# Kernel optimization log

Hardware: AMD Instinct MI355X
Metric: run time of the kernel (lower is better)

## Reference

```python
import jax, jax.numpy as jnp
import numpy as np

B, S, E, H = 2, 2048, 1024, 16
HD = E // H


def setup_inputs() -> dict:
    key = jax.random.key(0)
    ks = jax.random.split(key, 5)
    scale = 1.0 / np.sqrt(E)
    return {
        "query": jax.random.normal(ks[0], (B, S, E), jnp.float32),
        "key": jax.random.normal(ks[1], (B, S, E), jnp.float32),
        "value": jax.random.normal(ks[2], (B, S, E), jnp.float32),
        "qkv_w": jax.random.normal(ks[3], (3 * E, E), jnp.float32) * scale,
        "qkv_b": jnp.zeros((3 * E,), jnp.float32),
        "out_w": jax.random.normal(ks[4], (E, E), jnp.float32) * scale,
        "out_b": jnp.zeros((E,), jnp.float32),
    }


def reference(query, key, value, qkv_w, qkv_b, out_w, out_b):
    # Fused QKV projection from query (module ignores key/value contents)
    qkv = query @ qkv_w.T + qkv_b                      # [B,S,3E]
    qkv = qkv.reshape(B, S, 3, H, HD)
    q = qkv[:, :, 0].transpose(0, 2, 1, 3)             # [B,H,S,HD]
    k = qkv[:, :, 1].transpose(0, 2, 1, 3)
    v = qkv[:, :, 2].transpose(0, 2, 1, 3)
    scaling = 1.0 / np.sqrt(HD)
    scores = jnp.einsum("bhqd,bhkd->bhqk", q, k) * scaling  # [B,H,S,S]
    probs = jax.nn.softmax(scores, axis=-1)
    ctx = jnp.einsum("bhqk,bhkd->bhqd", probs, v)      # [B,H,S,HD]
    ctx = ctx.transpose(0, 2, 1, 3).reshape(B, S, E)
    return ctx @ out_w.T + out_b
```

## Files before the change

kernel.cpp:

```cpp
#include <hip/hip_runtime.h>
#include <hip/hip_bf16.h>
#include <math.h>

#define BB 2
#define SS 2048
#define EE 1024
#define HH 16
#define HD 64

typedef __bf16 bf16;
typedef __bf16 bf16x8 __attribute__((ext_vector_type(8)));
typedef float floatx4 __attribute__((ext_vector_type(4)));
typedef float floatx16 __attribute__((ext_vector_type(16)));

#define MFMA(a, b, c) __builtin_amdgcn_mfma_f32_16x16x32_bf16(a, b, c, 0, 0, 0)
#define MFMA32(a, b, c) __builtin_amdgcn_mfma_f32_32x32x16_bf16(a, b, c, 0, 0, 0)

__device__ inline void async16(const bf16* g, bf16* l) {
    __builtin_amdgcn_global_load_lds(
        (const __attribute__((address_space(1))) void*)g,
        (__attribute__((address_space(3))) void*)l, 16, 0, 0);
}

__device__ inline unsigned cvt_pk_bf16(float a, float b) {
    unsigned r;
    asm("v_cvt_pk_bf16_f32 %0, %1, %2" : "=v"(r) : "v"(a), "v"(b));
    return r;
}

__device__ inline float fast_exp2(float x) {
    float r;
    asm("v_exp_f32 %0, %1" : "=v"(r) : "v"(x));
    return r;
}

__global__ __launch_bounds__(256) void cvt3(
    const float* __restrict__ a, const float* __restrict__ b,
    const float* __restrict__ c,
    bf16* __restrict__ oa, bf16* __restrict__ ob, bf16* __restrict__ oc) {
    const long NA = (long)4096 * 1024, NB = (long)3072 * 1024, NC = (long)1024 * 1024;
    const long total = (NA + NB + NC) >> 2;
    long i = (long)blockIdx.x * blockDim.x + threadIdx.x;
    const long stride = (long)gridDim.x * blockDim.x;
    for (; i < total; i += stride) {
        const long e = i << 2;
        const float* src;
        bf16* dst;
        if (e < NA)           { src = a + e;            dst = oa + e; }
        else if (e < NA + NB) { src = b + (e - NA);     dst = ob + (e - NA); }
        else                  { src = c + (e - NA - NB); dst = oc + (e - NA - NB); }
        float4 v = *(const float4*)src;
        union { bf16 h[4]; uint2 u; } t;
        t.h[0] = (bf16)v.x; t.h[1] = (bf16)v.y; t.h[2] = (bf16)v.z; t.h[3] = (bf16)v.w;
        *(uint2*)dst = t.u;
    }
}

__global__ __launch_bounds__(256) void qkv_gemm(
    const bf16* __restrict__ A, const bf16* __restrict__ W,
    const float* __restrict__ bias,
    bf16* __restrict__ Qw, bf16* __restrict__ Kw, bf16* __restrict__ Vtw) {
    __shared__ __align__(16) bf16 As[2][128 * 64];
    __shared__ __align__(16) bf16 Bs[2][128 * 64];
    const int tid  = threadIdx.x;
    const int wave = tid >> 6, lane = tid & 63;
    const int quad = lane >> 4, l16 = lane & 15;
    const int wr = wave >> 1, wc = wave & 1;
    const int m0 = blockIdx.y * 128, n0 = blockIdx.x * 128;
    const int lr = lane >> 3;
    const int lcs = ((lane & 7) ^ (lr & 7)) * 8;
    const int rsw = (l16 & 7) << 3;

    const bf16* Ag = A + (long)(m0 + wave * 32 + lr) * 1024 + lcs;
    const bf16* Bg = W + (long)(n0 + wave * 32 + lr) * 1024 + lcs;
    const int lbase = (wave * 32) * 64 + lane * 8;

    floatx4 acc[4][4] = {};

#pragma unroll
    for (int j = 0; j < 4; ++j) {
        async16(Ag + (long)j * 8 * 1024, &As[0][lbase + j * 8 * 64]);
        async16(Bg + (long)j * 8 * 1024, &Bs[0][lbase + j * 8 * 64]);
    }

    for (int ks = 0; ks < 16; ++ks) {
        __syncthreads();
        const int cur = ks & 1;
        if (ks < 15) {
            const int nxt = cur ^ 1, k0 = (ks + 1) * 64;
#pragma unroll
            for (int j = 0; j < 4; ++j) {
                async16(Ag + (long)j * 8 * 1024 + k0, &As[nxt][lbase + j * 8 * 64]);
                async16(Bg + (long)j * 8 * 1024 + k0, &Bs[nxt][lbase + j * 8 * 64]);
            }
        }
#pragma unroll
        for (int c = 0; c < 2; ++c) {
            bf16x8 af[4], bfr[4];
#pragma unroll
            for (int mi = 0; mi < 4; ++mi)
                af[mi] = *(const bf16x8*)&As[cur][(wr * 64 + mi * 16 + l16) * 64 + ((c * 32 + quad * 8) ^ rsw)];
#pragma unroll
            for (int ni = 0; ni < 4; ++ni)
                bfr[ni] = *(const bf16x8*)&Bs[cur][(wc * 64 + ni * 16 + l16) * 64 + ((c * 32 + quad * 8) ^ rsw)];
#pragma unroll
            for (int mi = 0; mi < 4; ++mi)
#pragma unroll
                for (int ni = 0; ni < 4; ++ni)
                    acc[mi][ni] = MFMA(af[mi], bfr[ni], acc[mi][ni]);
        }
    }

#pragma unroll
    for (int mi = 0; mi < 4; ++mi)
#pragma unroll
        for (int ni = 0; ni < 4; ++ni) {
            const int n = n0 + wc * 64 + ni * 16 + l16;
            const float bn = bias[n];
            const int sel = n >> 10;
            const int e = n & 1023, h = e >> 6, d = e & 63;
            if (sel == 2) {
                const int m_base = m0 + wr * 64 + mi * 16 + quad * 4;
                const int b = m_base >> 11, s0 = m_base & 2047;
                union { bf16 h4[4]; uint2 u; } t;
#pragma unroll
                for (int r = 0; r < 4; ++r)
                    t.h4[r] = (bf16)(acc[mi][ni][r] + bn);
                *(uint2*)&Vtw[((long)(b * HH + h) * HD + d) * SS + s0] = t.u;
            } else {
#pragma unroll
                for (int r = 0; r < 4; ++r) {
                    const int m = m0 + wr * 64 + mi * 16 + quad * 4 + r;
                    const int b = m >> 11, s = m & 2047;
                    const float v = acc[mi][ni][r] + bn;
                    if (sel == 0)
                        Qw[((long)(b * HH + h) * SS + s) * HD + d] = (bf16)(v * 0.18033688f);
                    else
                        Kw[((long)(b * HH + h) * SS + s) * HD + d] = (bf16)v;
                }
            }
        }
}

__global__ __launch_bounds__(256) void attn(
    const bf16* __restrict__ Qw, const bf16* __restrict__ Kw,
    const bf16* __restrict__ Vtw, bf16* __restrict__ ctxw) {
    __shared__ __align__(16) bf16 Kts[2][64 * 64];
    __shared__ __align__(16) bf16 Vts[2][64 * 64];

    const int tid = threadIdx.x;
    const int wave = tid >> 6, lane = tid & 63;
    const int l5 = lane & 31, hi = lane >> 5;

    const int d_  = blockIdx.y * gridDim.x + blockIdx.x;
    const int j_  = d_ >> 3;
    const int bh  = (d_ & 7) * 4 + (j_ >> 4);
    const int qb  = j_ & 15;

    const bf16* Qh = Qw  + (long)bh * SS * HD;
    const bf16* Kh = Kw  + (long)bh * SS * HD;
    const bf16* Vh = Vtw + (long)bh * HD * SS;

    const int qbase = qb * 128 + wave * 32;
    bf16x8 qf[4];
#pragma unroll
    for (int d0 = 0; d0 < 4; ++d0)
        qf[d0] = *(const bf16x8*)&Qh[(long)(qbase + l5) * HD + d0 * 16 + hi * 8];

    floatx16 ctx0 = {}, ctx1 = {};
    float lsum = 0.f;

    const int wrow = wave * 8 + (lane >> 3);
    const int sch  = ((lane & 7) ^ ((lane >> 3) & 7)) * 8;
    const bf16* Kg0 = Kh + (long)wrow * HD + sch;
    const bf16* Kg1 = Kh + (long)(32 + wrow) * HD + sch;
    const bf16* Vg0 = Vh + (long)wrow * SS + sch;
    const bf16* Vg1 = Vh + (long)(32 + wrow) * SS + sch;
    const int ldst = wave * 512 + lane * 8;
    const int rswz = (l5 & 7) << 3;

    async16(Kg0, &Kts[0][ldst]);
    async16(Kg1, &Kts[0][ldst + 2048]);
    async16(Vg0, &Vts[0][ldst]);
    async16(Vg1, &Vts[0][ldst + 2048]);

    for (int kt = 0; kt < 32; ++kt) {
        __syncthreads();

        if (kt < 31) {
            const int nb = (kt + 1) & 1;
            const long ko = (long)(kt + 1) * 64;
            async16(Kg0 + ko * HD, &Kts[nb][ldst]);
            async16(Kg1 + ko * HD, &Kts[nb][ldst + 2048]);
            async16(Vg0 + ko,      &Vts[nb][ldst]);
            async16(Vg1 + ko,      &Vts[nb][ldst + 2048]);
        }
        const bf16* Kc = Kts[kt & 1];
        const bf16* Vc = Vts[kt & 1];

        floatx16 sf[2];
#pragma unroll
        for (int kb = 0; kb < 2; ++kb) {
            floatx16 s = {};
            __builtin_amdgcn_s_setprio(1);
#pragma unroll
            for (int d0 = 0; d0 < 4; ++d0) {
                const bf16x8 af = *(const bf16x8*)
                    &Kc[(kb * 32 + l5) * 64 + ((d0 * 16 + hi * 8) ^ rswz)];
                s = MFMA32(af, qf[d0], s);
            }
            __builtin_amdgcn_s_setprio(0);
            sf[kb] = s;
        }

#pragma unroll
        for (int kb = 0; kb < 2; ++kb) {
#pragma unroll
            for (int r = 0; r < 16; ++r) {
                const float p = fast_exp2(sf[kb][r]);
                sf[kb][r] = p;
                lsum += p;
            }
            unsigned w[8];
#pragma unroll
            for (int i = 0; i < 8; ++i)
                w[i] = cvt_pk_bf16(sf[kb][2 * i], sf[kb][2 * i + 1]);
            asm("v_permlane32_swap_b32 %0, %1" : "+v"(w[0]), "+v"(w[2]));
            asm("v_permlane32_swap_b32 %0, %1" : "+v"(w[1]), "+v"(w[3]));
            asm("v_permlane32_swap_b32 %0, %1" : "+v"(w[4]), "+v"(w[6]));
            asm("v_permlane32_swap_b32 %0, %1" : "+v"(w[5]), "+v"(w[7]));
            union { unsigned u[4]; bf16x8 v; } pa0 = {{w[0], w[1], w[2], w[3]}},
                                               pa1 = {{w[4], w[5], w[6], w[7]}};
#pragma unroll
            for (int kc = 0; kc < 2; ++kc) {
                const bf16x8 pa = kc ? pa1.v : pa0.v;
                const int kcol = kb * 32 + kc * 16 + hi * 8;
                const bf16x8 vf0 = *(const bf16x8*)&Vc[l5 * 64 + (kcol ^ rswz)];
                const bf16x8 vf1 = *(const bf16x8*)&Vc[(32 + l5) * 64 + (kcol ^ rswz)];
                __builtin_amdgcn_s_setprio(1);
                ctx0 = MFMA32(pa, vf0, ctx0);
                ctx1 = MFMA32(pa, vf1, ctx1);
                __builtin_amdgcn_s_setprio(0);
            }
        }
    }

    const float rs  = lsum + __shfl_xor(lsum, 32, 64);
    const float inv = 1.0f / rs;

    const int b = bh >> 4, h = bh & 15;
#pragma unroll
    for (int r = 0; r < 16; ++r) {
        const int qrow = (r & 3) + 8 * (r >> 2) + 4 * hi;
        const float iq = __shfl(inv, qrow, 64);
        const long base = ((long)b * SS + qbase + qrow) * EE + h * HD;
        ctxw[base + l5]      = (bf16)(ctx0[r] * iq);
        ctxw[base + 32 + l5] = (bf16)(ctx1[r] * iq);
    }
}

__global__ __launch_bounds__(256) void out_gemm(
    const bf16* __restrict__ A, const bf16* __restrict__ W,
    const float* __restrict__ bias, float* __restrict__ out) {
    __shared__ __align__(16) bf16 As[2][64 * 64];
    __shared__ __align__(16) bf16 Bs[2][128 * 64];
    const int tid  = threadIdx.x;
    const int wave = tid >> 6, lane = tid & 63;
    const int quad = lane >> 4, l16 = lane & 15;
    const int wr = wave & 1, wc = wave >> 1;
    const int m0 = blockIdx.y * 64, n0 = blockIdx.x * 128;
    const int lr = lane >> 3;
    const int lcs = ((lane & 7) ^ (lr & 7)) * 8;
    const int rsw = (l16 & 7) << 3;

    const bf16* Ag = A + (long)(m0 + wave * 16 + lr) * 1024 + lcs;
    const bf16* Bg = W + (long)(n0 + wave * 32 + lr) * 1024 + lcs;
    const int labase = (wave * 16) * 64 + lane * 8;
    const int lbbase = (wave * 32) * 64 + lane * 8;

    floatx4 acc[2][4] = {};

#pragma unroll
    for (int j = 0; j < 2; ++j)
        async16(Ag + (long)j * 8 * 1024, &As[0][labase + j * 8 * 64]);
#pragma unroll
    for (int j = 0; j < 4; ++j)
        async16(Bg + (long)j * 8 * 1024, &Bs[0][lbbase + j * 8 * 64]);

    for (int ks = 0; ks < 16; ++ks) {
        __syncthreads();
        const int cur = ks & 1;
        if (ks < 15) {
            const int nxt = cur ^ 1, k0 = (ks + 1) * 64;
#pragma unroll
            for (int j = 0; j < 2; ++j)
                async16(Ag + (long)j * 8 * 1024 + k0, &As[nxt][labase + j * 8 * 64]);
#pragma unroll
            for (int j = 0; j < 4; ++j)
                async16(Bg + (long)j * 8 * 1024 + k0, &Bs[nxt][lbbase + j * 8 * 64]);
        }
#pragma unroll
        for (int c = 0; c < 2; ++c) {
            bf16x8 af[2], bfr[4];
#pragma unroll
            for (int mi = 0; mi < 2; ++mi)
                af[mi] = *(const bf16x8*)&As[cur][(wr * 32 + mi * 16 + l16) * 64 + ((c * 32 + quad * 8) ^ rsw)];
#pragma unroll
            for (int ni = 0; ni < 4; ++ni)
                bfr[ni] = *(const bf16x8*)&Bs[cur][(wc * 64 + ni * 16 + l16) * 64 + ((c * 32 + quad * 8) ^ rsw)];
#pragma unroll
            for (int mi = 0; mi < 2; ++mi)
#pragma unroll
                for (int ni = 0; ni < 4; ++ni)
                    acc[mi][ni] = MFMA(af[mi], bfr[ni], acc[mi][ni]);
        }
    }

#pragma unroll
    for (int mi = 0; mi < 2; ++mi)
#pragma unroll
        for (int ni = 0; ni < 4; ++ni) {
            const int n = n0 + wc * 64 + ni * 16 + l16;
            const float bn = bias[n];
#pragma unroll
            for (int r = 0; r < 4; ++r) {
                const int m = m0 + wr * 32 + mi * 16 + quad * 4 + r;
                out[(long)m * 1024 + n] = acc[mi][ni][r] + bn;
            }
        }
}

extern "C" void kernel_launch(void* const* d_in, const int* in_sizes, int n_in,
                              void* d_out, int out_size, void* d_ws, size_t ws_size,
                              hipStream_t stream) {
    const float* query = (const float*)d_in[0];
    const float* qkv_w = (const float*)d_in[3];
    const float* qkv_b = (const float*)d_in[4];
    const float* out_w = (const float*)d_in[5];
    const float* out_b = (const float*)d_in[6];

    const long NTOK = (long)BB * SS;
    bf16* qb   = (bf16*)d_ws;
    bf16* wqb  = qb  + NTOK * EE;
    bf16* owb  = wqb + (long)3 * EE * EE;
    bf16* Qw   = owb + (long)EE * EE;
    bf16* Kw   = Qw  + NTOK * EE;
    bf16* Vtw  = Kw  + NTOK * EE;
    bf16* ctxw = qb;
    float* out = (float*)d_out;

    cvt3<<<2048, 256, 0, stream>>>(query, qkv_w, out_w, qb, wqb, owb);
    qkv_gemm<<<dim3(24, 32), 256, 0, stream>>>(qb, wqb, qkv_b, Qw, Kw, Vtw);
    attn<<<dim3(16, 32), 256, 0, stream>>>(Qw, Kw, Vtw, ctxw);
    out_gemm<<<dim3(8, 64), 256, 0, stream>>>(ctxw, owb, out_b, out);
}
```

Before: 215.6 us.

## Split attention key range across two wave groups and reduce through LDS

```diff
diff --git a/kernel.cpp b/kernel.cpp
--- a/kernel.cpp
+++ b/kernel.cpp
@@ -142,14 +142,14 @@
         }
 }
 
-__global__ __launch_bounds__(256) void attn(
+__global__ __launch_bounds__(512) void attn(
     const bf16* __restrict__ Qw, const bf16* __restrict__ Kw,
     const bf16* __restrict__ Vtw, bf16* __restrict__ ctxw) {
-    __shared__ __align__(16) bf16 Kts[2][64 * 64];
-    __shared__ __align__(16) bf16 Vts[2][64 * 64];
+    extern __shared__ __align__(16) bf16 smem[];
 
     const int tid = threadIdx.x;
     const int wave = tid >> 6, lane = tid & 63;
+    const int grp = wave >> 2, w4 = wave & 3;
     const int l5 = lane & 31, hi = lane >> 5;
 
     const int d_  = blockIdx.y * gridDim.x + blockIdx.x;
@@ -161,7 +161,7 @@
     const bf16* Kh = Kw  + (long)bh * SS * HD;
     const bf16* Vh = Vtw + (long)bh * HD * SS;
 
-    const int qbase = qb * 128 + wave * 32;
+    const int qbase = qb * 128 + w4 * 32;
     bf16x8 qf[4];
 #pragma unroll
     for (int d0 = 0; d0 < 4; ++d0)
@@ -170,33 +170,40 @@
     floatx16 ctx0 = {}, ctx1 = {};
     float lsum = 0.f;
 
-    const int wrow = wave * 8 + (lane >> 3);
+    const int wrow = w4 * 8 + (lane >> 3);
     const int sch  = ((lane & 7) ^ ((lane >> 3) & 7)) * 8;
-    const bf16* Kg0 = Kh + (long)wrow * HD + sch;
-    const bf16* Kg1 = Kh + (long)(32 + wrow) * HD + sch;
-    const bf16* Vg0 = Vh + (long)wrow * SS + sch;
-    const bf16* Vg1 = Vh + (long)(32 + wrow) * SS + sch;
-    const int ldst = wave * 512 + lane * 8;
+    const int kvo  = grp * 1024;
+    const bf16* Kg0 = Kh + (long)(kvo + wrow) * HD + sch;
+    const bf16* Kg1 = Kh + (long)(kvo + 32 + wrow) * HD + sch;
+    const bf16* Vg0 = Vh + (long)wrow * SS + kvo + sch;
+    const bf16* Vg1 = Vh + (long)(32 + wrow) * SS + kvo + sch;
+    const int ldst = w4 * 512 + lane * 8;
     const int rswz = (l5 & 7) << 3;
 
-    async16(Kg0, &Kts[0][ldst]);
-    async16(Kg1, &Kts[0][ldst + 2048]);
-    async16(Vg0, &Vts[0][ldst]);
-    async16(Vg1, &Vts[0][ldst + 2048]);
-
-    for (int kt = 0; kt < 32; ++kt) {
+    bf16* Kt0 = smem + (grp * 2 + 0) * 4096;
+    bf16* Kt1 = smem + (grp * 2 + 1) * 4096;
+    bf16* Vt0 = smem + 16384 + (grp * 2 + 0) * 4096;
+    bf16* Vt1 = smem + 16384 + (grp * 2 + 1) * 4096;
+
+    async16(Kg0, Kt0 + ldst);
+    async16(Kg1, Kt0 + ldst + 2048);
+    async16(Vg0, Vt0 + ldst);
+    async16(Vg1, Vt0 + ldst + 2048);
+
+    for (int kt = 0; kt < 16; ++kt) {
         __syncthreads();
 
-        if (kt < 31) {
-            const int nb = (kt + 1) & 1;
+        if (kt < 15) {
+            bf16* Kn = (kt & 1) ? Kt0 : Kt1;
+            bf16* Vn = (kt & 1) ? Vt0 : Vt1;
             const long ko = (long)(kt + 1) * 64;
-            async16(Kg0 + ko * HD, &Kts[nb][ldst]);
-            async16(Kg1 + ko * HD, &Kts[nb][ldst + 2048]);
-            async16(Vg0 + ko,      &Vts[nb][ldst]);
-            async16(Vg1 + ko,      &Vts[nb][ldst + 2048]);
-        }
-        const bf16* Kc = Kts[kt & 1];
-        const bf16* Vc = Vts[kt & 1];
+            async16(Kg0 + ko * HD, Kn + ldst);
+            async16(Kg1 + ko * HD, Kn + ldst + 2048);
+            async16(Vg0 + ko,      Vn + ldst);
+            async16(Vg1 + ko,      Vn + ldst + 2048);
+        }
+        const bf16* Kc = (kt & 1) ? Kt1 : Kt0;
+        const bf16* Vc = (kt & 1) ? Vt1 : Vt0;
 
         floatx16 sf[2];
 #pragma unroll
@@ -245,17 +252,37 @@
         }
     }
 
-    const float rs  = lsum + __shfl_xor(lsum, 32, 64);
-    const float inv = 1.0f / rs;
-
-    const int b = bh >> 4, h = bh & 15;
-#pragma unroll
-    for (int r = 0; r < 16; ++r) {
-        const int qrow = (r & 3) + 8 * (r >> 2) + 4 * hi;
-        const float iq = __shfl(inv, qrow, 64);
-        const long base = ((long)b * SS + qbase + qrow) * EE + h * HD;
-        ctxw[base + l5]      = (bf16)(ctx0[r] * iq);
-        ctxw[base + 32 + l5] = (bf16)(ctx1[r] * iq);
+    __syncthreads();
+    float* cb = (float*)smem;
+    float* lb = (float*)(smem + 16384);
+    if (grp == 1) {
+#pragma unroll
+        for (int r = 0; r < 16; ++r) {
+            cb[(w4 * 32 + r) * 64 + lane]      = ctx0[r];
+            cb[(w4 * 32 + 16 + r) * 64 + lane] = ctx1[r];
+        }
+        lb[w4 * 64 + lane] = lsum;
+    }
+    __syncthreads();
+    if (grp == 0) {
+        lsum += lb[w4 * 64 + lane];
+#pragma unroll
+        for (int r = 0; r < 16; ++r) {
+            ctx0[r] += cb[(w4 * 32 + r) * 64 + lane];
+            ctx1[r] += cb[(w4 * 32 + 16 + r) * 64 + lane];
+        }
+        const float rs  = lsum + __shfl_xor(lsum, 32, 64);
+        const float inv = 1.0f / rs;
+
+        const int b = bh >> 4, h = bh & 15;
+#pragma unroll
+        for (int r = 0; r < 16; ++r) {
+            const int qrow = (r & 3) + 8 * (r >> 2) + 4 * hi;
+            const float iq = __shfl(inv, qrow, 64);
+            const long base = ((long)b * SS + qbase + qrow) * EE + h * HD;
+            ctxw[base + l5]      = (bf16)(ctx0[r] * iq);
+            ctxw[base + 32 + l5] = (bf16)(ctx1[r] * iq);
+        }
     }
 }
 
@@ -351,6 +378,6 @@
 
     cvt3<<<2048, 256, 0, stream>>>(query, qkv_w, out_w, qb, wqb, owb);
     qkv_gemm<<<dim3(24, 32), 256, 0, stream>>>(qb, wqb, qkv_b, Qw, Kw, Vtw);
-    attn<<<dim3(16, 32), 256, 0, stream>>>(Qw, Kw, Vtw, ctxw);
+    attn<<<dim3(16, 32), 512, 65536, stream>>>(Qw, Kw, Vtw, ctxw);
     out_gemm<<<dim3(8, 64), 256, 0, stream>>>(ctxw, owb, out_b, out);
 }
```

New measurement: 208.3 us. 3.4% less time.
